# Performance work log

Hardware: AMD Instinct MI355X
Metric: run time of the kernel (lower is better)

Reference implementation:

```python
import jax, jax.numpy as jnp
import numpy as np

N = 8192
F_IN = 1024
F_OUT = 512

def glorot(key, shape):
    limit = np.sqrt(6.0 / (shape[0] + shape[1]))
    return jax.random.uniform(key, shape, minval=-limit, maxval=limit, dtype=jnp.float32)

def setup_inputs() -> dict:
    key = jax.random.key(0)
    k1, k2, k3 = jax.random.split(key, 3)
    x = jax.random.normal(k1, (N, F_IN), dtype=jnp.float32)
    adj = jax.random.uniform(k2, (N, N), dtype=jnp.float32)  # dense nonnegative adjacency
    W = glorot(k3, (F_IN, F_OUT))
    b = jnp.zeros((F_OUT,), dtype=jnp.float32)
    return {"x": x, "adj": adj, "W": W, "b": b}

def reference(x, adj, W, b):
    # GCN layer: relu( D^{-1/2} (A + I) D^{-1/2} @ (x @ W) + b )
    n = adj.shape[0]
    A = adj + jnp.eye(n, dtype=adj.dtype)            # add self loops (tf.diag(In))
    d = jnp.sum(A, axis=1)                            # row-sum degrees
    d_is = d ** -0.5                                  # D^{-1/2}
    # D1 @ A @ D1 expressed as row/col scaling (identical math, no diag GEMMs)
    A_norm = A * d_is[:, None] * d_is[None, :]
    pre_sup = x @ W                                   # [N, F_OUT]
    out = A_norm @ pre_sup + b                        # propagation + bias
    return jax.nn.relu(out)
```

## Files before the change

### kernel.cpp

```cpp
#include <hip/hip_runtime.h>
#include <stdint.h>

#define NN 8192
#define FIN 1024
#define FOUT 512

typedef __attribute__((ext_vector_type(4))) float f32x4;
typedef __attribute__((ext_vector_type(8))) short s16x8;
typedef __attribute__((ext_vector_type(4))) unsigned short u16x4;

__device__ __forceinline__ short f2bf(float f) {
    return __builtin_bit_cast(short, static_cast<__bf16>(f));
}
__device__ __forceinline__ float bf2f(short s) {
    return (float)__builtin_bit_cast(__bf16, s);
}

__global__ __launch_bounds__(256) void rowsum_cvt_kernel(const float* __restrict__ adj,
                                                         short* __restrict__ adjB,
                                                         float* __restrict__ d_is) {
    const int row = blockIdx.x;
    const float4* a = reinterpret_cast<const float4*>(adj + (size_t)row * NN);
    u16x4* ob = reinterpret_cast<u16x4*>(adjB + (size_t)row * NN);
    float s = 0.f;
    #pragma unroll 2
    for (int j = threadIdx.x; j < NN / 4; j += 256) {
        float4 v = a[j];
        s += (v.x + v.y) + (v.z + v.w);
        u16x4 p;
        p[0] = (unsigned short)f2bf(v.x); p[1] = (unsigned short)f2bf(v.y);
        p[2] = (unsigned short)f2bf(v.z); p[3] = (unsigned short)f2bf(v.w);
        ob[j] = p;
    }
    #pragma unroll
    for (int off = 32; off > 0; off >>= 1) s += __shfl_down(s, off, 64);
    __shared__ float red[4];
    if ((threadIdx.x & 63) == 0) red[threadIdx.x >> 6] = s;
    __syncthreads();
    if (threadIdx.x == 0) {
        const float d = red[0] + red[1] + red[2] + red[3] + 1.0f;
        d_is[row] = 1.0f / sqrtf(d);
    }
}

__global__ __launch_bounds__(256) void rowsum_kernel(const float* __restrict__ adj,
                                                     float* __restrict__ d_is) {
    const int row = blockIdx.x;
    const float4* a = reinterpret_cast<const float4*>(adj + (size_t)row * NN);
    float s = 0.f;
    #pragma unroll 4
    for (int j = threadIdx.x; j < NN / 4; j += 256) {
        float4 v = a[j];
        s += (v.x + v.y) + (v.z + v.w);
    }
    #pragma unroll
    for (int off = 32; off > 0; off >>= 1) s += __shfl_down(s, off, 64);
    __shared__ float red[4];
    if ((threadIdx.x & 63) == 0) red[threadIdx.x >> 6] = s;
    __syncthreads();
    if (threadIdx.x == 0) {
        const float d = red[0] + red[1] + red[2] + red[3] + 1.0f;
        d_is[row] = 1.0f / sqrtf(d);
    }
}

__global__ __launch_bounds__(256) void cvt_x_kernel(const float* __restrict__ x,
                                                    short* __restrict__ xB) {
    const size_t i = ((size_t)blockIdx.x * 256 + threadIdx.x) * 8;
    const float4 v0 = *reinterpret_cast<const float4*>(&x[i]);
    const float4 v1 = *reinterpret_cast<const float4*>(&x[i + 4]);
    s16x8 o;
    o[0] = f2bf(v0.x); o[1] = f2bf(v0.y); o[2] = f2bf(v0.z); o[3] = f2bf(v0.w);
    o[4] = f2bf(v1.x); o[5] = f2bf(v1.y); o[6] = f2bf(v1.z); o[7] = f2bf(v1.w);
    *reinterpret_cast<s16x8*>(&xB[i]) = o;
}

__global__ __launch_bounds__(256) void wt_kernel(const float* __restrict__ W,
                                                 short* __restrict__ WT) {
    __shared__ float T[64][68];
    const int wc = blockIdx.x;
    const int wk = blockIdx.y;
    const int t = threadIdx.x;
    const int cc = (t & 15) * 4;
    #pragma unroll
    for (int i = 0; i < 4; ++i) {
        const int rr = (t >> 4) + i * 16;
        *reinterpret_cast<float4*>(&T[rr][cc]) =
            *reinterpret_cast<const float4*>(&W[(size_t)(wk * 64 + rr) * FOUT + wc * 64 + cc]);
    }
    __syncthreads();
    const int a = t >> 2;
    const int b0 = (t & 3) * 16;
    s16x8 v0, v1;
    #pragma unroll
    for (int e = 0; e < 8; ++e) { v0[e] = f2bf(T[b0 + e][a]); v1[e] = f2bf(T[b0 + 8 + e][a]); }
    short* dst = &WT[(size_t)(wc * 64 + a) * FIN + wk * 64 + b0];
    *reinterpret_cast<s16x8*>(dst) = v0;
    *reinterpret_cast<s16x8*>(dst + 8) = v1;
}

__global__ __launch_bounds__(256, 4) void xwg_kernel(const short* __restrict__ xB,
                                                     const short* __restrict__ WT,
                                                     const float* __restrict__ d_is,
                                                     short* __restrict__ psT) {
    constexpr int NT = FIN / 32;
    __shared__ short As[2][4096];
    __shared__ short Bs[2][2048];

    const int tid = threadIdx.x;
    const int lin = blockIdx.x;
    const int swz = (lin & 7) * 64 + (lin >> 3);
    const int col0 = (swz & 7) * 64;
    const int row0 = (swz >> 3) * 128;

    const int lane = tid & 63;
    const int wv = tid >> 6;
    const int wr = wv >> 1, wc = wv & 1;
    const int l15 = lane & 15;
    const int kq = lane >> 4;
    const int xorv = (l15 & 12) << 2;

    int arow[2], acoff[2];
    #pragma unroll
    for (int i = 0; i < 2; ++i) {
        const int slot = i * 256 + tid;
        const int P = (slot << 4) ^ (slot & 48);
        arow[i] = P >> 6;
        acoff[i] = (P & 63) >> 1;
    }
    const short* Ab = xB + (size_t)row0 * FIN;
    const short* Bb = WT + (size_t)col0 * FIN;

    auto stage = [&](int buf, int k0) {
        #pragma unroll
        for (int i = 0; i < 2; ++i) {
            const short* src = Ab + (size_t)arow[i] * FIN + k0 + acoff[i];
            short* dst = &As[buf][(i * 256 + (tid & 192)) * 8];
            __builtin_amdgcn_global_load_lds(
                (const __attribute__((address_space(1))) unsigned int*)src,
                (__attribute__((address_space(3))) unsigned int*)dst, 16, 0, 0);
        }
        {
            const short* src = Bb + (size_t)arow[0] * FIN + k0 + acoff[0];
            short* dst = &Bs[buf][(tid & 192) * 8];
            __builtin_amdgcn_global_load_lds(
                (const __attribute__((address_space(1))) unsigned int*)src,
                (__attribute__((address_space(3))) unsigned int*)dst, 16, 0, 0);
        }
    };

    f32x4 acc[4][2] = {};
    auto compute = [&](int buf) {
        s16x8 af[4], bfr[2];
        #pragma unroll
        for (int m = 0; m < 4; ++m) {
            const int byteoff = ((wr * 64 + m * 16 + l15) * 64 + kq * 16) ^ xorv;
            af[m] = *reinterpret_cast<const s16x8*>(&As[buf][byteoff >> 1]);
        }
        #pragma unroll
        for (int n = 0; n < 2; ++n) {
            const int byteoff = ((wc * 32 + n * 16 + l15) * 64 + kq * 16) ^ xorv;
            bfr[n] = *reinterpret_cast<const s16x8*>(&Bs[buf][byteoff >> 1]);
        }
        #pragma unroll
        for (int m = 0; m < 4; ++m)
            #pragma unroll
            for (int n = 0; n < 2; ++n)
                acc[m][n] = __builtin_amdgcn_mfma_f32_16x16x32_bf16(af[m], bfr[n], acc[m][n], 0, 0, 0);
    };

    stage(0, 0);
    stage(1, 32);
    int cur = 0;
    #pragma unroll 1
    for (int t = 0; t < NT; ++t) {
        if (t < NT - 1) {
            asm volatile("s_waitcnt vmcnt(3)" ::: "memory");
        } else {
            asm volatile("s_waitcnt vmcnt(0)" ::: "memory");
        }
        __builtin_amdgcn_s_barrier();
        compute(cur);
        if (t + 2 < NT) {
            __builtin_amdgcn_s_barrier();
            stage(cur, (t + 2) * 32);
        }
        cur ^= 1;
    }

    #pragma unroll
    for (int m = 0; m < 4; ++m) {
        const int rbase = row0 + wr * 64 + m * 16 + kq * 4;
        float dr[4];
        #pragma unroll
        for (int j = 0; j < 4; ++j) dr[j] = d_is[rbase + j];
        #pragma unroll
        for (int n = 0; n < 2; ++n) {
            const int col = col0 + wc * 32 + n * 16 + l15;
            u16x4 pk;
            #pragma unroll
            for (int j = 0; j < 4; ++j) pk[j] = (unsigned short)f2bf(dr[j] * acc[m][n][j]);
            *reinterpret_cast<u16x4*>(&psT[(size_t)col * NN + rbase]) = pk;
        }
    }
}

__global__ __launch_bounds__(256, 4) void prop2_kernel(
    const short* __restrict__ adjB, const short* __restrict__ psT,
    short* __restrict__ Pb0, short* __restrict__ Pb1,
    short* __restrict__ Pb2, float* __restrict__ Pf) {
    constexpr int Ksub = NN / 4;
    constexpr int NT = Ksub / 32;
    __shared__ short As[2][4096];
    __shared__ short Bs[2][4096];

    const int tid = threadIdx.x;
    const int lin = blockIdx.x;
    const int swz = (lin & 7) * 128 + (lin >> 3);
    const int col0 = (swz & 3) * 128;
    const int ks = (swz >> 2) & 3;
    const int row0 = (swz >> 4) * 128;

    const int lane = tid & 63;
    const int wv = tid >> 6;
    const int wr = wv >> 1, wc = wv & 1;
    const int l15 = lane & 15;
    const int kq = lane >> 4;
    const int xorv = (l15 & 12) << 2;

    int arow[2], acoff[2];
    #pragma unroll
    for (int i = 0; i < 2; ++i) {
        const int slot = i * 256 + tid;
        const int P = (slot << 4) ^ (slot & 48);
        arow[i] = P >> 6;
        acoff[i] = (P & 63) >> 1;
    }
    const size_t kbase = (size_t)ks * Ksub;
    const short* Ab = adjB + (size_t)row0 * NN + kbase;
    const short* Bb = psT + (size_t)col0 * NN + kbase;

    auto stage = [&](int buf, int k0) {
        #pragma unroll
        for (int i = 0; i < 2; ++i) {
            const short* src = Ab + (size_t)arow[i] * NN + k0 + acoff[i];
            short* dst = &As[buf][(i * 256 + (tid & 192)) * 8];
            __builtin_amdgcn_global_load_lds(
                (const __attribute__((address_space(1))) unsigned int*)src,
                (__attribute__((address_space(3))) unsigned int*)dst, 16, 0, 0);
        }
        #pragma unroll
        for (int i = 0; i < 2; ++i) {
            const short* src = Bb + (size_t)arow[i] * NN + k0 + acoff[i];
            short* dst = &Bs[buf][(i * 256 + (tid & 192)) * 8];
            __builtin_amdgcn_global_load_lds(
                (const __attribute__((address_space(1))) unsigned int*)src,
                (__attribute__((address_space(3))) unsigned int*)dst, 16, 0, 0);
        }
    };

    f32x4 acc[4][4] = {};
    auto compute = [&](int buf) {
        s16x8 af[4], bfr[4];
        #pragma unroll
        for (int m = 0; m < 4; ++m) {
            const int byteoff = ((wr * 64 + m * 16 + l15) * 64 + kq * 16) ^ xorv;
            af[m] = *reinterpret_cast<const s16x8*>(&As[buf][byteoff >> 1]);
        }
        #pragma unroll
        for (int n = 0; n < 4; ++n) {
            const int byteoff = ((wc * 64 + n * 16 + l15) * 64 + kq * 16) ^ xorv;
            bfr[n] = *reinterpret_cast<const s16x8*>(&Bs[buf][byteoff >> 1]);
        }
        #pragma unroll
        for (int m = 0; m < 4; ++m)
            #pragma unroll
            for (int n = 0; n < 4; ++n)
                acc[m][n] = __builtin_amdgcn_mfma_f32_16x16x32_bf16(af[m], bfr[n], acc[m][n], 0, 0, 0);
    };

    stage(0, 0);
    stage(1, 32);
    int cur = 0;
    #pragma unroll 1
    for (int t = 0; t < NT; ++t) {
        if (t < NT - 1) {
            asm volatile("s_waitcnt vmcnt(4)" ::: "memory");
        } else {
            asm volatile("s_waitcnt vmcnt(0)" ::: "memory");
        }
        __builtin_amdgcn_s_barrier();
        compute(cur);
        if (t + 2 < NT) {
            __builtin_amdgcn_s_barrier();
            stage(cur, (t + 2) * 32);
        }
        cur ^= 1;
    }

    if (ks == 3) {
        #pragma unroll
        for (int m = 0; m < 4; ++m) {
            const int rbase = row0 + wr * 64 + m * 16 + kq * 4;
            #pragma unroll
            for (int n = 0; n < 4; ++n) {
                const int col = col0 + wc * 64 + n * 16 + l15;
                #pragma unroll
                for (int j = 0; j < 4; ++j)
                    Pf[(size_t)(rbase + j) * FOUT + col] = acc[m][n][j];
            }
        }
    } else {
        short* Pt = (ks == 0) ? Pb0 : (ks == 1) ? Pb1 : Pb2;
        #pragma unroll
        for (int m = 0; m < 4; ++m) {
            const int rbase = row0 + wr * 64 + m * 16 + kq * 4;
            #pragma unroll
            for (int n = 0; n < 4; ++n) {
                const int col = col0 + wc * 64 + n * 16 + l15;
                #pragma unroll
                for (int j = 0; j < 4; ++j)
                    Pt[(size_t)(rbase + j) * FOUT + col] = f2bf(acc[m][n][j]);
            }
        }
    }
}

__global__ __launch_bounds__(256) void ep4_kernel(
    const short* __restrict__ Pb0, const short* __restrict__ Pb1,
    const short* __restrict__ Pb2, float* __restrict__ out,
    const short* __restrict__ psT, const float* __restrict__ d_is,
    const float* __restrict__ bias) {
    const int col0 = blockIdx.x * 128;
    const int row0 = blockIdx.y * 32;
    const int t = threadIdx.x;
    const int c = col0 + (t & 31) * 4;
    const float4 bb = *reinterpret_cast<const float4*>(&bias[c]);
    #pragma unroll
    for (int it = 0; it < 4; ++it) {
        const int r = row0 + (t >> 5) + it * 8;
        const size_t idx = (size_t)r * FOUT + c;
        const u16x4 a = *reinterpret_cast<const u16x4*>(&Pb0[idx]);
        const u16x4 b4 = *reinterpret_cast<const u16x4*>(&Pb1[idx]);
        const u16x4 c4 = *reinterpret_cast<const u16x4*>(&Pb2[idx]);
        const float4 d4 = *reinterpret_cast<const float4*>(&out[idx]);
        const float dr = d_is[r];
        float s[4], o4[4];
        #pragma unroll
        for (int j = 0; j < 4; ++j) s[j] = bf2f(psT[(size_t)(c + j) * NN + r]);
        const float dd[4] = {d4.x, d4.y, d4.z, d4.w};
        const float bbv[4] = {bb.x, bb.y, bb.z, bb.w};
        #pragma unroll
        for (int j = 0; j < 4; ++j) {
            const float sum = ((bf2f((short)a[j]) + bf2f((short)b4[j])) +
                               (bf2f((short)c4[j]) + dd[j])) + s[j];
            o4[j] = fmaxf(dr * sum + bbv[j], 0.f);
        }
        float4 o = {o4[0], o4[1], o4[2], o4[3]};
        *reinterpret_cast<float4*>(&out[idx]) = o;
    }
}

template<int KLEN, int MODE>
__global__ __launch_bounds__(256, 4) void gemm_kernel(
    const float* __restrict__ A, const short* __restrict__ B,
    const float* __restrict__ d_is,
    short* __restrict__ psT,
    float* __restrict__ P0, float* __restrict__ P1) {
    constexpr int KS = (MODE == 1) ? 2 : 1;
    constexpr int Ksub = KLEN / KS;
    constexpr int NT = Ksub / 32;
    constexpr int LDA = 40;
    __shared__ short As[2][128 * LDA];
    __shared__ short Bs[2][64 * LDA];

    const int tid = threadIdx.x;
    const int nchunk = gridDim.x >> 3;
    const int lin = blockIdx.x;
    const int swz = (lin & 7) * nchunk + (lin >> 3);
    const int col0 = (swz & 7) * 64;
    const int yp = (swz >> 3) & 63;
    const int ks = swz >> 9;
    const int row0 = yp * 128;
    const int kbase = ks * Ksub;

    const int lane = tid & 63;
    const int wv = tid >> 6;
    const int wr = wv >> 1, wc = wv & 1;
    const int l15 = lane & 15;
    const int koff = (lane >> 4) * 8;

    const int ar = tid >> 1, ak = (tid & 1) * 16;
    const float* Abase = A + (size_t)(row0 + ar) * KLEN + kbase + ak;
    const int br = tid >> 2, bk = (tid & 3) * 8;
    const short* Bbase = B + (size_t)(col0 + br) * KLEN + kbase + bk;

    float4 qa0, qa1, qa2, qa3;
    s16x8 qb;
    auto loadG = [&](int k0) {
        const float4* p = reinterpret_cast<const float4*>(Abase + k0);
        qa0 = p[0]; qa1 = p[1]; qa2 = p[2]; qa3 = p[3];
        qb = *reinterpret_cast<const s16x8*>(Bbase + k0);
    };
    auto writeL = [&](int buf) {
        const float a[16] = {qa0.x, qa0.y, qa0.z, qa0.w, qa1.x, qa1.y, qa1.z, qa1.w,
                             qa2.x, qa2.y, qa2.z, qa2.w, qa3.x, qa3.y, qa3.z, qa3.w};
        s16x8 v0, v1;
        #pragma unroll
        for (int e = 0; e < 8; ++e) { v0[e] = f2bf(a[e]); v1[e] = f2bf(a[8 + e]); }
        *reinterpret_cast<s16x8*>(&As[buf][ar * LDA + ak]) = v0;
        *reinterpret_cast<s16x8*>(&As[buf][ar * LDA + ak + 8]) = v1;
        *reinterpret_cast<s16x8*>(&Bs[buf][br * LDA + bk]) = qb;
    };

    f32x4 acc[4][2] = {};
    auto compute = [&](int buf) {
        s16x8 af[4], bfr[2];
        #pragma unroll
        for (int m = 0; m < 4; ++m)
            af[m] = *reinterpret_cast<const s16x8*>(&As[buf][(wr * 64 + m * 16 + l15) * LDA + koff]);
        #pragma unroll
        for (int n = 0; n < 2; ++n)
            bfr[n] = *reinterpret_cast<const s16x8*>(&Bs[buf][(wc * 32 + n * 16 + l15) * LDA + koff]);
        #pragma unroll
        for (int m = 0; m < 4; ++m)
            #pragma unroll
            for (int n = 0; n < 2; ++n)
                acc[m][n] = __builtin_amdgcn_mfma_f32_16x16x32_bf16(af[m], bfr[n], acc[m][n], 0, 0, 0);
    };

    loadG(0);
    writeL(0);
    __syncthreads();
    int cur = 0;
    for (int t = 0; t < NT; ++t) {
        if (t + 1 < NT) loadG((t + 1) * 32);
        compute(cur);
        if (t + 1 < NT) writeL(cur ^ 1);
        __syncthreads();
        cur ^= 1;
    }

    if (MODE == 0) {
        #pragma unroll
        for (int m = 0; m < 4; ++m) {
            const int rbase = row0 + wr * 64 + m * 16 + (lane >> 4) * 4;
            float dr[4];
            #pragma unroll
            for (int j = 0; j < 4; ++j) dr[j] = d_is[rbase + j];
            #pragma unroll
            for (int n = 0; n < 2; ++n) {
                const int col = col0 + wc * 32 + n * 16 + l15;
                u16x4 pk;
                #pragma unroll
                for (int j = 0; j < 4; ++j) pk[j] = (unsigned short)f2bf(dr[j] * acc[m][n][j]);
                *reinterpret_cast<u16x4*>(&psT[(size_t)col * NN + rbase]) = pk;
            }
        }
    } else {
        float* tgt = (ks == 0) ? P0 : P1;
        #pragma unroll
        for (int m = 0; m < 4; ++m) {
            const int rbase = row0 + wr * 64 + m * 16 + (lane >> 4) * 4;
            #pragma unroll
            for (int n = 0; n < 2; ++n) {
                const int col = col0 + wc * 32 + n * 16 + l15;
                f32x4 v = acc[m][n];
                if (ks == 0) {
                    const u16x4 sv = *reinterpret_cast<const u16x4*>(&psT[(size_t)col * NN + rbase]);
                    #pragma unroll
                    for (int j = 0; j < 4; ++j) v[j] += bf2f((short)sv[j]);
                }
                #pragma unroll
                for (int j = 0; j < 4; ++j)
                    tgt[(size_t)(rbase + j) * FOUT + col] = v[j];
            }
        }
    }
}

__global__ __launch_bounds__(256) void ep_kernel(const float* __restrict__ P0,
                                                 float* __restrict__ out,
                                                 const float* __restrict__ d_is,
                                                 const float* __restrict__ bias) {
    const size_t idx = ((size_t)blockIdx.x * 256 + threadIdx.x) * 4;
    const int row = (int)(idx >> 9);
    const int col = (int)(idx & 511);
    const float4 p0 = *reinterpret_cast<const float4*>(&P0[idx]);
    const float4 p1 = *reinterpret_cast<const float4*>(&out[idx]);
    const float4 bb = *reinterpret_cast<const float4*>(&bias[col]);
    const float dr = d_is[row];
    float4 o;
    o.x = fmaxf(dr * (p0.x + p1.x) + bb.x, 0.f);
    o.y = fmaxf(dr * (p0.y + p1.y) + bb.y, 0.f);
    o.z = fmaxf(dr * (p0.z + p1.z) + bb.z, 0.f);
    o.w = fmaxf(dr * (p0.w + p1.w) + bb.w, 0.f);
    *reinterpret_cast<float4*>(&out[idx]) = o;
}

extern "C" void kernel_launch(void* const* d_in, const int* in_sizes, int n_in,
                              void* d_out, int out_size, void* d_ws, size_t ws_size,
                              hipStream_t stream) {
    const float* x   = (const float*)d_in[0];
    const float* adj = (const float*)d_in[1];
    const float* W   = (const float*)d_in[2];
    const float* b   = (const float*)d_in[3];
    float* out = (float*)d_out;

    const size_t NEED = (size_t)FOUT * NN * 2 + (size_t)FOUT * FIN * 2
                      + (size_t)NN * FIN * 2 + 3ull * NN * FOUT * 2
                      + NN * 4 + (size_t)NN * NN * 2;

    if (ws_size >= NEED) {
        short* psT = (short*)d_ws;
        short* WT  = psT + (size_t)FOUT * NN;
        short* xB  = WT + (size_t)FOUT * FIN;
        short* Pb0 = xB + (size_t)NN * FIN;
        short* Pb1 = Pb0 + (size_t)NN * FOUT;
        short* Pb2 = Pb1 + (size_t)NN * FOUT;
        float* dis = (float*)(Pb2 + (size_t)NN * FOUT);
        short* adjB = (short*)(dis + NN);

        hipLaunchKernelGGL(rowsum_cvt_kernel, dim3(NN), dim3(256), 0, stream, adj, adjB, dis);
        hipLaunchKernelGGL(cvt_x_kernel, dim3(NN * FIN / 2048), dim3(256), 0, stream, x, xB);
        hipLaunchKernelGGL(wt_kernel, dim3(8, 16), dim3(256), 0, stream, W, WT);
        hipLaunchKernelGGL(xwg_kernel, dim3(512), dim3(256), 0, stream, xB, WT, dis, psT);
        hipLaunchKernelGGL(prop2_kernel, dim3(1024), dim3(256), 0, stream,
                           adjB, psT, Pb0, Pb1, Pb2, out);
        hipLaunchKernelGGL(ep4_kernel, dim3(4, 256), dim3(256), 0, stream,
                           Pb0, Pb1, Pb2, out, psT, dis, b);
    } else {
        short* psT = (short*)d_ws;
        short* WT  = psT + (size_t)FOUT * NN;
        float* P0  = (float*)(WT + (size_t)FOUT * FIN);
        float* dis = P0 + (size_t)NN * FOUT;

        hipLaunchKernelGGL(rowsum_kernel, dim3(NN), dim3(256), 0, stream, adj, dis);
        hipLaunchKernelGGL(wt_kernel, dim3(8, 16), dim3(256), 0, stream, W, WT);
        hipLaunchKernelGGL((gemm_kernel<FIN, 0>), dim3(512), dim3(256), 0, stream,
                           x, WT, dis, psT, nullptr, nullptr);
        hipLaunchKernelGGL((gemm_kernel<NN, 1>), dim3(1024), dim3(256), 0, stream,
                           adj, psT, dis, psT, P0, out);
        hipLaunchKernelGGL(ep_kernel, dim3(NN * FOUT / 1024), dim3(256), 0, stream,
                           P0, out, dis, b);
    }
}
```

Measured before the change: 218.1 us.

## Enlarge propagation GEMM to 256x256 tiles with phased pipelining; fuse prep kernels

Replaces the 128x128-tile, 256-thread propagation GEMM with a 256x256-tile, 512-thread kernel. It uses 128KB of dynamic LDS, double-buffers 64-wide K slices split into half-phases, and interleaves global-to-LDS staging with MFMA compute behind barriers and s_setprio. The larger tile raises arithmetic intensity and cuts redundant adjacency and feature traffic, at the cost of one block per CU and only 256 blocks. The three preprocessing kernels (adjacency row-sum/convert, x convert, W transpose) are also merged into one launch to remove launch gaps.

```diff
diff --git a/kernel.cpp b/kernel.cpp
--- a/kernel.cpp
+++ b/kernel.cpp
@@ -16,30 +16,67 @@
     return (float)__builtin_bit_cast(__bf16, s);
 }
 
-__global__ __launch_bounds__(256) void rowsum_cvt_kernel(const float* __restrict__ adj,
-                                                         short* __restrict__ adjB,
-                                                         float* __restrict__ d_is) {
-    const int row = blockIdx.x;
-    const float4* a = reinterpret_cast<const float4*>(adj + (size_t)row * NN);
-    u16x4* ob = reinterpret_cast<u16x4*>(adjB + (size_t)row * NN);
-    float s = 0.f;
-    #pragma unroll 2
-    for (int j = threadIdx.x; j < NN / 4; j += 256) {
-        float4 v = a[j];
-        s += (v.x + v.y) + (v.z + v.w);
-        u16x4 p;
-        p[0] = (unsigned short)f2bf(v.x); p[1] = (unsigned short)f2bf(v.y);
-        p[2] = (unsigned short)f2bf(v.z); p[3] = (unsigned short)f2bf(v.w);
-        ob[j] = p;
-    }
-    #pragma unroll
-    for (int off = 32; off > 0; off >>= 1) s += __shfl_down(s, off, 64);
+__global__ __launch_bounds__(256) void prep_kernel(const float* __restrict__ adj,
+                                                   short* __restrict__ adjB,
+                                                   float* __restrict__ d_is,
+                                                   const float* __restrict__ x,
+                                                   short* __restrict__ xB,
+                                                   const float* __restrict__ W,
+                                                   short* __restrict__ WT) {
     __shared__ float red[4];
-    if ((threadIdx.x & 63) == 0) red[threadIdx.x >> 6] = s;
-    __syncthreads();
-    if (threadIdx.x == 0) {
-        const float d = red[0] + red[1] + red[2] + red[3] + 1.0f;
-        d_is[row] = 1.0f / sqrtf(d);
+    __shared__ float T[64][68];
+    const int b = blockIdx.x;
+    const int t = threadIdx.x;
+    if (b < NN) {
+        const int row = b;
+        const float4* a = reinterpret_cast<const float4*>(adj + (size_t)row * NN);
+        u16x4* ob = reinterpret_cast<u16x4*>(adjB + (size_t)row * NN);
+        float s = 0.f;
+        #pragma unroll 2
+        for (int j = t; j < NN / 4; j += 256) {
+            float4 v = a[j];
+            s += (v.x + v.y) + (v.z + v.w);
+            u16x4 p;
+            p[0] = (unsigned short)f2bf(v.x); p[1] = (unsigned short)f2bf(v.y);
+            p[2] = (unsigned short)f2bf(v.z); p[3] = (unsigned short)f2bf(v.w);
+            ob[j] = p;
+        }
+        #pragma unroll
+        for (int off = 32; off > 0; off >>= 1) s += __shfl_down(s, off, 64);
+        if ((t & 63) == 0) red[t >> 6] = s;
+        __syncthreads();
+        if (t == 0) {
+            const float d = red[0] + red[1] + red[2] + red[3] + 1.0f;
+            d_is[row] = 1.0f / sqrtf(d);
+        }
+    } else if (b < NN + 4096) {
+        const size_t i = ((size_t)(b - NN) * 256 + t) * 8;
+        const float4 v0 = *reinterpret_cast<const float4*>(&x[i]);
+        const float4 v1 = *reinterpret_cast<const float4*>(&x[i + 4]);
+        s16x8 o;
+        o[0] = f2bf(v0.x); o[1] = f2bf(v0.y); o[2] = f2bf(v0.z); o[3] = f2bf(v0.w);
+        o[4] = f2bf(v1.x); o[5] = f2bf(v1.y); o[6] = f2bf(v1.z); o[7] = f2bf(v1.w);
+        *reinterpret_cast<s16x8*>(&xB[i]) = o;
+    } else {
+        const int bid = b - NN - 4096;
+        const int wc = bid & 7;
+        const int wk = bid >> 3;
+        const int cc = (t & 15) * 4;
+        #pragma unroll
+        for (int i = 0; i < 4; ++i) {
+            const int rr = (t >> 4) + i * 16;
+            *reinterpret_cast<float4*>(&T[rr][cc]) =
+                *reinterpret_cast<const float4*>(&W[(size_t)(wk * 64 + rr) * FOUT + wc * 64 + cc]);
+        }
+        __syncthreads();
+        const int a = t >> 2;
+        const int b0 = (t & 3) * 16;
+        s16x8 v0, v1;
+        #pragma unroll
+        for (int e = 0; e < 8; ++e) { v0[e] = f2bf(T[b0 + e][a]); v1[e] = f2bf(T[b0 + 8 + e][a]); }
+        short* dst = &WT[(size_t)(wc * 64 + a) * FIN + wk * 64 + b0];
+        *reinterpret_cast<s16x8*>(dst) = v0;
+        *reinterpret_cast<s16x8*>(dst + 8) = v1;
     }
 }
 
@@ -64,17 +101,6 @@
     }
 }
 
-__global__ __launch_bounds__(256) void cvt_x_kernel(const float* __restrict__ x,
-                                                    short* __restrict__ xB) {
-    const size_t i = ((size_t)blockIdx.x * 256 + threadIdx.x) * 8;
-    const float4 v0 = *reinterpret_cast<const float4*>(&x[i]);
-    const float4 v1 = *reinterpret_cast<const float4*>(&x[i + 4]);
-    s16x8 o;
-    o[0] = f2bf(v0.x); o[1] = f2bf(v0.y); o[2] = f2bf(v0.z); o[3] = f2bf(v0.w);
-    o[4] = f2bf(v1.x); o[5] = f2bf(v1.y); o[6] = f2bf(v1.z); o[7] = f2bf(v1.w);
-    *reinterpret_cast<s16x8*>(&xB[i]) = o;
-}
-
 __global__ __launch_bounds__(256) void wt_kernel(const float* __restrict__ W,
                                                  short* __restrict__ WT) {
     __shared__ float T[64][68];
@@ -205,125 +231,143 @@
     }
 }
 
-__global__ __launch_bounds__(256, 4) void prop2_kernel(
+__global__ __launch_bounds__(512, 1) void prop3_kernel(
     const short* __restrict__ adjB, const short* __restrict__ psT,
     short* __restrict__ Pb0, short* __restrict__ Pb1,
     short* __restrict__ Pb2, float* __restrict__ Pf) {
-    constexpr int Ksub = NN / 4;
-    constexpr int NT = Ksub / 32;
-    __shared__ short As[2][4096];
-    __shared__ short Bs[2][4096];
+    extern __shared__ short L[];
 
     const int tid = threadIdx.x;
     const int lin = blockIdx.x;
-    const int swz = (lin & 7) * 128 + (lin >> 3);
-    const int col0 = (swz & 3) * 128;
-    const int ks = (swz >> 2) & 3;
-    const int row0 = (swz >> 4) * 128;
+    const int swz = (lin & 7) * 32 + (lin >> 3);
+    const int col0 = (swz & 1) * 256;
+    const int ks = (swz >> 1) & 3;
+    const int row0 = (swz >> 3) * 256;
 
     const int lane = tid & 63;
     const int wv = tid >> 6;
-    const int wr = wv >> 1, wc = wv & 1;
+    const int wr = wv >> 2;
+    const int wc = wv & 3;
     const int l15 = lane & 15;
     const int kq = lane >> 4;
     const int xorv = (l15 & 12) << 2;
 
-    int arow[2], acoff[2];
+    int srow[2], scol[2];
     #pragma unroll
     for (int i = 0; i < 2; ++i) {
-        const int slot = i * 256 + tid;
+        const int slot = i * 512 + tid;
         const int P = (slot << 4) ^ (slot & 48);
-        arow[i] = P >> 6;
-        acoff[i] = (P & 63) >> 1;
-    }
-    const size_t kbase = (size_t)ks * Ksub;
+        srow[i] = P >> 6;
+        scol[i] = (P & 63) >> 1;
+    }
+    const size_t kbase = (size_t)ks * 2048;
     const short* Ab = adjB + (size_t)row0 * NN + kbase;
     const short* Bb = psT + (size_t)col0 * NN + kbase;
 
-    auto stage = [&](int buf, int k0) {
+    auto stageH = [&](int buf, int op, int kh, int t) {
+        const short* s0 = op ? Bb : Ab;
+        const int k0 = t * 64 + kh * 32;
+        short* base = &L[buf * 32768 + op * 16384 + kh * 8192];
         #pragma unroll
         for (int i = 0; i < 2; ++i) {
-            const short* src = Ab + (size_t)arow[i] * NN + k0 + acoff[i];
-            short* dst = &As[buf][(i * 256 + (tid & 192)) * 8];
+            const short* src = s0 + (size_t)srow[i] * NN + k0 + scol[i];
+            short* dst = base + (i * 512 + (tid & 448)) * 8;
             __builtin_amdgcn_global_load_lds(
                 (const __attribute__((address_space(1))) unsigned int*)src,
                 (__attribute__((address_space(3))) unsigned int*)dst, 16, 0, 0);
         }
-        #pragma unroll
-        for (int i = 0; i < 2; ++i) {
-            const short* src = Bb + (size_t)arow[i] * NN + k0 + acoff[i];
-            short* dst = &Bs[buf][(i * 256 + (tid & 192)) * 8];
-            __builtin_amdgcn_global_load_lds(
-                (const __attribute__((address_space(1))) unsigned int*)src,
-                (__attribute__((address_space(3))) unsigned int*)dst, 16, 0, 0);
-        }
     };
 
-    f32x4 acc[4][4] = {};
-    auto compute = [&](int buf) {
-        s16x8 af[4], bfr[4];
-        #pragma unroll
-        for (int m = 0; m < 4; ++m) {
-            const int byteoff = ((wr * 64 + m * 16 + l15) * 64 + kq * 16) ^ xorv;
-            af[m] = *reinterpret_cast<const s16x8*>(&As[buf][byteoff >> 1]);
-        }
-        #pragma unroll
-        for (int n = 0; n < 4; ++n) {
-            const int byteoff = ((wc * 64 + n * 16 + l15) * 64 + kq * 16) ^ xorv;
-            bfr[n] = *reinterpret_cast<const s16x8*>(&Bs[buf][byteoff >> 1]);
-        }
-        #pragma unroll
-        for (int m = 0; m < 4; ++m)
-            #pragma unroll
-            for (int n = 0; n < 4; ++n)
-                acc[m][n] = __builtin_amdgcn_mfma_f32_16x16x32_bf16(af[m], bfr[n], acc[m][n], 0, 0, 0);
-    };
-
-    stage(0, 0);
-    stage(1, 32);
-    int cur = 0;
+    f32x4 acc[8][4] = {};
+
+#define LDFRAG(BASE, ROW) \
+    (*reinterpret_cast<const s16x8*>(&(BASE)[((((ROW) * 64 + kq * 16)) ^ xorv) >> 1]))
+
+#define PHASE(BUF, KH, QM, STAGE_STMT, VM_STMT)                                     \
+    do {                                                                            \
+        const short* Ah_ = &L[(BUF) * 32768 + (KH) * 8192];                         \
+        const short* Bh_ = &L[(BUF) * 32768 + 16384 + (KH) * 8192];                 \
+        s16x8 af_[4], bg_[4];                                                       \
+        _Pragma("unroll")                                                           \
+        for (int m = 0; m < 4; ++m)                                                 \
+            af_[m] = LDFRAG(Ah_, wr * 128 + (QM) * 64 + m * 16 + l15);              \
+        _Pragma("unroll")                                                           \
+        for (int n = 0; n < 4; ++n)                                                 \
+            bg_[n] = LDFRAG(Bh_, wc * 64 + n * 16 + l15);                           \
+        STAGE_STMT;                                                                 \
+        asm volatile("" ::: "memory");                                              \
+        __builtin_amdgcn_s_barrier();                                               \
+        __builtin_amdgcn_s_setprio(1);                                              \
+        _Pragma("unroll")                                                           \
+        for (int m = 0; m < 4; ++m)                                                 \
+            _Pragma("unroll")                                                       \
+            for (int n = 0; n < 4; ++n)                                             \
+                acc[(QM) * 4 + m][n] = __builtin_amdgcn_mfma_f32_16x16x32_bf16(     \
+                    af_[m], bg_[n], acc[(QM) * 4 + m][n], 0, 0, 0);                 \
+        __builtin_amdgcn_s_setprio(0);                                              \
+        VM_STMT;                                                                    \
+        asm volatile("" ::: "memory");                                              \
+        __builtin_amdgcn_s_barrier();                                               \
+    } while (0)
+
+#define VM4 asm volatile("s_waitcnt vmcnt(4)" ::: "memory")
+#define VM0 asm volatile("s_waitcnt vmcnt(0)" ::: "memory")
+
+    stageH(0, 0, 0, 0); stageH(0, 1, 0, 0);
+    stageH(0, 0, 1, 0); stageH(0, 1, 1, 0);
+    stageH(1, 0, 0, 1); stageH(1, 1, 0, 1);
+    asm volatile("s_waitcnt vmcnt(8)" ::: "memory");
+    __builtin_amdgcn_s_barrier();
+
+    PHASE(0, 0, 0, (void)0,             (void)0);
+    PHASE(0, 0, 1, (void)0,             VM4);
+    PHASE(0, 1, 0, stageH(1, 0, 1, 1),  (void)0);
+    PHASE(0, 1, 1, stageH(1, 1, 1, 1),  VM4);
+
     #pragma unroll 1
-    for (int t = 0; t < NT; ++t) {
-        if (t < NT - 1) {
-            asm volatile("s_waitcnt vmcnt(4)" ::: "memory");
-        } else {
-            asm volatile("s_waitcnt vmcnt(0)" ::: "memory");
-        }
-        __builtin_amdgcn_s_barrier();
-        compute(cur);
-        if (t + 2 < NT) {
-            __builtin_amdgcn_s_barrier();
-            stage(cur, (t + 2) * 32);
-        }
-        cur ^= 1;
-    }
+    for (int t = 1; t <= 30; ++t) {
+        const int buf = t & 1, nb = buf ^ 1, tn = t + 1;
+        PHASE(buf, 0, 0, stageH(nb, 0, 0, tn), (void)0);
+        PHASE(buf, 0, 1, stageH(nb, 1, 0, tn), VM4);
+        PHASE(buf, 1, 0, stageH(nb, 0, 1, tn), (void)0);
+        PHASE(buf, 1, 1, stageH(nb, 1, 1, tn), VM4);
+    }
+
+    PHASE(1, 0, 0, (void)0, (void)0);
+    PHASE(1, 0, 1, (void)0, VM0);
+    PHASE(1, 1, 0, (void)0, (void)0);
+    PHASE(1, 1, 1, (void)0, (void)0);
 
     if (ks == 3) {
         #pragma unroll
-        for (int m = 0; m < 4; ++m) {
-            const int rbase = row0 + wr * 64 + m * 16 + kq * 4;
+        for (int mi = 0; mi < 8; ++mi) {
+            const int rbase = row0 + wr * 128 + mi * 16 + kq * 4;
             #pragma unroll
             for (int n = 0; n < 4; ++n) {
                 const int col = col0 + wc * 64 + n * 16 + l15;
                 #pragma unroll
                 for (int j = 0; j < 4; ++j)
-                    Pf[(size_t)(rbase + j) * FOUT + col] = acc[m][n][j];
+                    Pf[(size_t)(rbase + j) * FOUT + col] = acc[mi][n][j];
             }
         }
     } else {
         short* Pt = (ks == 0) ? Pb0 : (ks == 1) ? Pb1 : Pb2;
         #pragma unroll
-        for (int m = 0; m < 4; ++m) {
-            const int rbase = row0 + wr * 64 + m * 16 + kq * 4;
+        for (int mi = 0; mi < 8; ++mi) {
+            const int rbase = row0 + wr * 128 + mi * 16 + kq * 4;
             #pragma unroll
             for (int n = 0; n < 4; ++n) {
                 const int col = col0 + wc * 64 + n * 16 + l15;
                 #pragma unroll
                 for (int j = 0; j < 4; ++j)
-                    Pt[(size_t)(rbase + j) * FOUT + col] = f2bf(acc[m][n][j]);
+                    Pt[(size_t)(rbase + j) * FOUT + col] = f2bf(acc[mi][n][j]);
             }
         }
     }
+#undef PHASE
+#undef LDFRAG
+#undef VM4
+#undef VM0
 }
 
 __global__ __launch_bounds__(256) void ep4_kernel(
@@ -521,11 +565,10 @@
         float* dis = (float*)(Pb2 + (size_t)NN * FOUT);
         short* adjB = (short*)(dis + NN);
 
-        hipLaunchKernelGGL(rowsum_cvt_kernel, dim3(NN), dim3(256), 0, stream, adj, adjB, dis);
-        hipLaunchKernelGGL(cvt_x_kernel, dim3(NN * FIN / 2048), dim3(256), 0, stream, x, xB);
-        hipLaunchKernelGGL(wt_kernel, dim3(8, 16), dim3(256), 0, stream, W, WT);
+        hipLaunchKernelGGL(prep_kernel, dim3(NN + 4096 + 128), dim3(256), 0, stream,
+                           adj, adjB, dis, x, xB, W, WT);
         hipLaunchKernelGGL(xwg_kernel, dim3(512), dim3(256), 0, stream, xB, WT, dis, psT);
-        hipLaunchKernelGGL(prop2_kernel, dim3(1024), dim3(256), 0, stream,
+        hipLaunchKernelGGL(prop3_kernel, dim3(256), dim3(512), 131072, stream,
                            adjB, psT, Pb0, Pb1, Pb2, out);
         hipLaunchKernelGGL(ep4_kernel, dim3(4, 256), dim3(256), 0, stream,
                            Pb0, Pb1, Pb2, out, psT, dis, b);
```

Result: faster. 192.0 us (-12.0%).
